# Kernel tuning notes

Measured on AMD Instinct MI355X. Metric: run time of the kernel, lower is better.

The kernel has to match this reference:

```python
import jax, jax.numpy as jnp
import numpy as np

N, H, F, E, K = 2048, 1024, 4096, 8, 2


def setup_inputs() -> dict:
    key = jax.random.key(0)
    ks = jax.random.split(key, 6)
    x = jax.random.normal(ks[0], (N, H), dtype=jnp.float32)
    mapping = jax.random.randint(ks[1], (N, K), 0, E)
    Wg = jax.random.normal(ks[2], (E, H), dtype=jnp.float32) * (1.0 / np.sqrt(H))
    W1 = jax.random.normal(ks[3], (E, H, F), dtype=jnp.float32) * (1.0 / np.sqrt(H))
    b1 = jnp.zeros((E, F), dtype=jnp.float32)
    W2 = jax.random.normal(ks[4], (E, F, H), dtype=jnp.float32) * (1.0 / np.sqrt(F))
    b2 = jnp.zeros((E, H), dtype=jnp.float32)
    return {"x": x, "mapping": mapping, "Wg": Wg, "W1": W1, "b1": b1, "W2": W2, "b2": b2}


def reference(x, mapping, Wg, W1, b1, W2, b2):
    # Gate logits: note original applies softmax over dim=0 (the token axis).
    logits = jax.nn.softmax(x @ Wg.T, axis=0)  # [N, E]

    # Per-expert MLP. Original sorts tokens by expert, runs per-expert GEMMs on
    # dynamic splits, then unsorts -- mathematically: y[i,k] = MLP_{mapping[i,k]}(x[i]).
    # JIT-friendly dense baseline: run every expert over all tokens, gather per token.
    def mlp(e):
        h = jax.nn.gelu(x @ W1[e] + b1[e])  # [N, F]
        return h @ W2[e] + b2[e]            # [N, H]

    y_all = jnp.stack([mlp(e) for e in range(E)])  # [E, N, H]

    # Gate weights gathered per (token, k), normalized over top-k.
    w = jnp.take_along_axis(logits, mapping, axis=1)  # [N, K]
    w = w / jnp.sum(w, axis=-1, keepdims=True)

    idx = jnp.arange(x.shape[0])
    out = jnp.zeros_like(x)
    for k in range(mapping.shape[1]):
        yk = y_all[mapping[:, k], idx]  # [N, H] gather per token's k-th expert
        out = out + yk * w[:, k:k + 1]
    return out
```

## Files before the change

### kernel.cpp

```cpp
#include <hip/hip_runtime.h>

#define N_TOK 2048
#define HD    1024
#define FD    4096
#define NE    8

typedef __attribute__((ext_vector_type(8))) short short8;
typedef __attribute__((ext_vector_type(4))) float floatx4;

__device__ __forceinline__ unsigned short f2bf(float f) {
  unsigned int u = __float_as_uint(f);
  u += 0x7fffu + ((u >> 16) & 1u);
  return (unsigned short)(u >> 16);
}

__device__ __forceinline__ void gl2lds16(const unsigned short* g, unsigned short* l) {
  __builtin_amdgcn_global_load_lds(
      (const __attribute__((address_space(1))) unsigned int*)g,
      (__attribute__((address_space(3))) unsigned int*)l, 16, 0, 0);
}

__device__ __forceinline__ float gelu_tanh(float x) {
  float t = 0.7978845608028654f * x * (1.0f + 0.044715f * x * x);
  return 0.5f * x * (1.0f + tanhf(t));
}

__device__ __forceinline__ int poff_of(const int* __restrict__ cnt, int e) {
  int o = 0;
  for (int i = 0; i < e; ++i) o += (cnt[i] + 127) & ~127;
  return o;
}

__global__ void k_gating(const float* __restrict__ x, const float* __restrict__ wg,
                         float* __restrict__ p) {
  int wave = threadIdx.x >> 6;
  int lane = threadIdx.x & 63;
  int n = blockIdx.x * 4 + wave;
  const float4* xr = (const float4*)(x + (size_t)n * HD);
  float4 xv[4];
  #pragma unroll
  for (int i = 0; i < 4; ++i) xv[i] = xr[lane + i * 64];
  for (int e = 0; e < NE; ++e) {
    const float4* wr = (const float4*)(wg + (size_t)e * HD);
    float s = 0.f;
    #pragma unroll
    for (int i = 0; i < 4; ++i) {
      float4 w4 = wr[lane + i * 64];
      s += xv[i].x * w4.x + xv[i].y * w4.y + xv[i].z * w4.z + xv[i].w * w4.w;
    }
    for (int o = 32; o > 0; o >>= 1) s += __shfl_xor(s, o, 64);
    if (lane == 0) p[e * N_TOK + n] = s;
  }
}

__global__ void k_softmax(float* __restrict__ p) {
  int e = blockIdx.x;
  float* col = p + e * N_TOK;
  __shared__ float red[256];
  int t = threadIdx.x;
  float m = -1e30f;
  for (int i = t; i < N_TOK; i += 256) m = fmaxf(m, col[i]);
  red[t] = m; __syncthreads();
  for (int s = 128; s > 0; s >>= 1) { if (t < s) red[t] = fmaxf(red[t], red[t + s]); __syncthreads(); }
  m = red[0]; __syncthreads();
  float sum = 0.f;
  for (int i = t; i < N_TOK; i += 256) { float v = expf(col[i] - m); col[i] = v; sum += v; }
  red[t] = sum; __syncthreads();
  for (int s = 128; s > 0; s >>= 1) { if (t < s) red[t] += red[t + s]; __syncthreads(); }
  float inv = 1.0f / red[0];
  for (int i = t; i < N_TOK; i += 256) col[i] *= inv;
}

__global__ void k_route(const int* __restrict__ mp, const float* __restrict__ p,
                        int* __restrict__ cnt, int* __restrict__ idxl,
                        int* __restrict__ tke, int* __restrict__ tks, float* __restrict__ tkw) {
  int n = blockIdx.x * 256 + threadIdx.x;
  if (n >= N_TOK) return;
  int m0 = mp[n * 2 + 0], m1 = mp[n * 2 + 1];
  if (m0 == m1) {
    int s = atomicAdd(&cnt[m0], 1);
    idxl[m0 * N_TOK + s] = n;
    tke[n * 2] = m0; tks[n * 2] = s; tkw[n * 2] = 1.0f;
    tke[n * 2 + 1] = m0; tks[n * 2 + 1] = s; tkw[n * 2 + 1] = 0.0f;
  } else {
    float p0 = p[m0 * N_TOK + n], p1 = p[m1 * N_TOK + n];
    float inv = 1.0f / (p0 + p1);
    int s0 = atomicAdd(&cnt[m0], 1);
    idxl[m0 * N_TOK + s0] = n;
    tke[n * 2] = m0; tks[n * 2] = s0; tkw[n * 2] = p0 * inv;
    int s1 = atomicAdd(&cnt[m1], 1);
    idxl[m1 * N_TOK + s1] = n;
    tke[n * 2 + 1] = m1; tks[n * 2 + 1] = s1; tkw[n * 2 + 1] = p1 * inv;
  }
}

__global__ void k_gather(const float* __restrict__ x, const int* __restrict__ cnt,
                         const int* __restrict__ idxl, unsigned short* __restrict__ xg) {
  int e = blockIdx.y;
  int r = blockIdx.x;
  int c = cnt[e];
  int pc = (c + 127) & ~127;
  if (r >= pc) return;
  unsigned short* dst = xg + ((size_t)poff_of(cnt, e) + r) * HD;
  int t = threadIdx.x;
  union { unsigned short us[8]; uint4 v; } o;
  if (r < c) {
    const float* src = x + (size_t)idxl[e * N_TOK + r] * HD;
    float4 f0 = ((const float4*)src)[t * 2];
    float4 f1 = ((const float4*)src)[t * 2 + 1];
    o.us[0] = f2bf(f0.x); o.us[1] = f2bf(f0.y); o.us[2] = f2bf(f0.z); o.us[3] = f2bf(f0.w);
    o.us[4] = f2bf(f1.x); o.us[5] = f2bf(f1.y); o.us[6] = f2bf(f1.z); o.us[7] = f2bf(f1.w);
  } else {
    o.v.x = 0u; o.v.y = 0u; o.v.z = 0u; o.v.w = 0u;
  }
  ((uint4*)dst)[t] = o.v;
}

__global__ __launch_bounds__(256) void k_transcvt2(const float* __restrict__ w1,
                                                   unsigned short* __restrict__ w1t,
                                                   const float* __restrict__ w2,
                                                   unsigned short* __restrict__ w2t) {
  __shared__ float tile[64][65];
  int l = blockIdx.x;
  const float* src; unsigned short* dst; int rows, cols, bx, by, e;
  if (l < 8192) {
    src = w1; dst = w1t; rows = HD; cols = FD;
    bx = l & 63; by = (l >> 6) & 15; e = l >> 10;
  } else {
    int l2 = l - 8192;
    src = w2; dst = w2t; rows = FD; cols = HD;
    bx = l2 & 15; by = (l2 >> 4) & 63; e = l2 >> 10;
  }
  const size_t base = (size_t)e * rows * cols;
  int c0 = bx * 64, r0 = by * 64;
  int t = threadIdx.x;
  int lr = t >> 4;
  int lc = (t & 15) * 4;
  #pragma unroll
  for (int i = 0; i < 64; i += 16) {
    float4 v = *(const float4*)(src + base + (size_t)(r0 + lr + i) * cols + c0 + lc);
    tile[lr + i][lc] = v.x; tile[lr + i][lc + 1] = v.y;
    tile[lr + i][lc + 2] = v.z; tile[lr + i][lc + 3] = v.w;
  }
  __syncthreads();
  int oc = t >> 2;
  int rseg = (t & 3) * 16;
  union { unsigned short us[16]; uint4 v[2]; } o;
  #pragma unroll
  for (int i = 0; i < 16; ++i) o.us[i] = f2bf(tile[rseg + i][oc]);
  unsigned short* d = dst + base + (size_t)(c0 + oc) * rows + r0 + rseg;
  ((uint4*)d)[0] = o.v[0];
  ((uint4*)d)[1] = o.v[1];
}

__global__ __launch_bounds__(256) void k_gemm1(
    const unsigned short* __restrict__ xg, const unsigned short* __restrict__ w1t,
    const float* __restrict__ b1, const int* __restrict__ cnt,
    unsigned short* __restrict__ h) {
  const int l = blockIdx.x;
  const int r = l & 7;
  const int m = (l >> 3) & 31;
  const int q = l >> 8;
  const int e = q >> 2;
  const int n = ((q & 3) << 3) | r;

  const int c = cnt[e];
  const int mbase = m * 64;
  if (mbase >= c) return;
  const int nbase = n * 128;
  const int po = poff_of(cnt, e);
  const unsigned short* A = xg + ((size_t)po + mbase) * HD;
  const unsigned short* B = w1t + ((size_t)e * FD + nbase) * HD;

  __shared__ unsigned short As[64 * 32];
  __shared__ unsigned short Bs[128 * 32];

  const int tid = threadIdx.x;
  const int wave = tid >> 6, lane = tid & 63;
  const int quad = lane >> 4, lrow = lane & 15;
  const int wn = wave * 32;

  floatx4 acc[4][2];
  #pragma unroll
  for (int i = 0; i < 4; ++i)
    #pragma unroll
    for (int j = 0; j < 2; ++j) acc[i][j] = (floatx4){0.f, 0.f, 0.f, 0.f};

  const int rA = tid >> 2, kA = (tid & 3) * 8;
  const int rB0 = tid >> 2, kB0 = (tid & 3) * 8;
  const int rB1 = (256 + tid) >> 2, kB1 = ((256 + tid) & 3) * 8;

  for (int kt = 0; kt < HD / 32; ++kt) {
    __syncthreads();
    const unsigned short* ga = A + kt * 32;
    const unsigned short* gb = B + kt * 32;
    gl2lds16(ga + (size_t)rA * HD + kA, As + (size_t)(wave * 64) * 8);
    gl2lds16(gb + (size_t)rB0 * HD + kB0, Bs + (size_t)(wave * 64) * 8);
    gl2lds16(gb + (size_t)rB1 * HD + kB1, Bs + (size_t)(256 + wave * 64) * 8);
    __syncthreads();
    short8 aF[4], bF[2];
    #pragma unroll
    for (int i = 0; i < 4; ++i) aF[i] = *(const short8*)(As + (i * 16 + lrow) * 32 + quad * 8);
    #pragma unroll
    for (int j = 0; j < 2; ++j) bF[j] = *(const short8*)(Bs + (wn + j * 16 + lrow) * 32 + quad * 8);
    #pragma unroll
    for (int i = 0; i < 4; ++i)
      #pragma unroll
      for (int j = 0; j < 2; ++j)
        acc[i][j] = __builtin_amdgcn_mfma_f32_16x16x32_bf16(aF[i], bF[j], acc[i][j], 0, 0, 0);
  }

  const size_t hrow0 = (size_t)po + mbase;
  #pragma unroll
  for (int i = 0; i < 4; ++i) {
    #pragma unroll
    for (int rr = 0; rr < 4; ++rr) {
      int row = i * 16 + quad * 4 + rr;
      unsigned short* hr = h + (hrow0 + row) * FD + nbase;
      #pragma unroll
      for (int j = 0; j < 2; ++j) {
        int col = wn + j * 16 + lrow;
        float v = acc[i][j][rr] + b1[e * FD + nbase + col];
        hr[col] = f2bf(gelu_tanh(v));
      }
    }
  }
}

__global__ __launch_bounds__(256) void k_gemm2(
    const unsigned short* __restrict__ h, const unsigned short* __restrict__ w2t,
    const int* __restrict__ cnt, unsigned short* __restrict__ ya) {
  const int l = blockIdx.x;
  const int nt = l & 15;
  const int mt = l >> 4;
  const int mbase = mt * 64;
  const int nbase = nt * 64;

  int e = -1, po = 0, ce = 0;
  {
    int o = 0;
    #pragma unroll
    for (int i = 0; i < NE; ++i) {
      int ci = cnt[i];
      int pc = (ci + 127) & ~127;
      if (mbase >= o && mbase < o + pc) { e = i; po = o; ce = ci; }
      o += pc;
    }
  }
  if (e < 0) return;
  if (mbase - po >= ce) return;

  const unsigned short* A = h + (size_t)mbase * FD;
  const unsigned short* B = w2t + ((size_t)e * HD + nbase) * FD;

  __shared__ unsigned short As[64 * 64];
  __shared__ unsigned short Bs[64 * 64];

  const int tid = threadIdx.x;
  const int wave = tid >> 6, lane = tid & 63;
  const int quad = lane >> 4, lrow = lane & 15;
  const int wm = (wave >> 1) * 32, wn = (wave & 1) * 32;

  floatx4 acc[2][2];
  #pragma unroll
  for (int i = 0; i < 2; ++i)
    #pragma unroll
    for (int j = 0; j < 2; ++j) acc[i][j] = (floatx4){0.f, 0.f, 0.f, 0.f};

  const int s0 = tid,        r0 = s0 >> 3, k0 = (s0 & 7) * 8;
  const int s1 = 256 + tid,  r1 = s1 >> 3, k1 = (s1 & 7) * 8;

  for (int kt = 0; kt < FD / 64; ++kt) {
    __syncthreads();
    const unsigned short* ga = A + kt * 64;
    const unsigned short* gb = B + kt * 64;
    gl2lds16(ga + (size_t)r0 * FD + k0, As + (size_t)(wave * 64) * 8);
    gl2lds16(ga + (size_t)r1 * FD + k1, As + (size_t)(256 + wave * 64) * 8);
    gl2lds16(gb + (size_t)r0 * FD + k0, Bs + (size_t)(wave * 64) * 8);
    gl2lds16(gb + (size_t)r1 * FD + k1, Bs + (size_t)(256 + wave * 64) * 8);
    __syncthreads();
    #pragma unroll
    for (int c = 0; c < 2; ++c) {
      short8 aF[2], bF[2];
      #pragma unroll
      for (int i = 0; i < 2; ++i) aF[i] = *(const short8*)(As + (wm + i * 16 + lrow) * 64 + c * 32 + quad * 8);
      #pragma unroll
      for (int j = 0; j < 2; ++j) bF[j] = *(const short8*)(Bs + (wn + j * 16 + lrow) * 64 + c * 32 + quad * 8);
      #pragma unroll
      for (int i = 0; i < 2; ++i)
        #pragma unroll
        for (int j = 0; j < 2; ++j)
          acc[i][j] = __builtin_amdgcn_mfma_f32_16x16x32_bf16(aF[i], bF[j], acc[i][j], 0, 0, 0);
    }
  }

  #pragma unroll
  for (int i = 0; i < 2; ++i) {
    #pragma unroll
    for (int rr = 0; rr < 4; ++rr) {
      int row = mbase + wm + i * 16 + quad * 4 + rr;
      unsigned short* yr = ya + (size_t)row * HD + nbase;
      #pragma unroll
      for (int j = 0; j < 2; ++j) {
        int col = wn + j * 16 + lrow;
        yr[col] = f2bf(acc[i][j][rr]);
      }
    }
  }
}

__global__ __launch_bounds__(256) void k_combine(
    const unsigned short* __restrict__ ya, const float* __restrict__ b2,
    const int* __restrict__ cnt, const int* __restrict__ tke,
    const int* __restrict__ tks, const float* __restrict__ tkw,
    float* __restrict__ out) {
  int n = blockIdx.x;
  int e0 = tke[n * 2], e1 = tke[n * 2 + 1];
  int p0 = poff_of(cnt, e0) + tks[n * 2];
  int p1 = poff_of(cnt, e1) + tks[n * 2 + 1];
  float w0 = tkw[n * 2], w1 = tkw[n * 2 + 1];
  int c = threadIdx.x * 4;
  union { unsigned short us[4]; ushort2 u2[2]; unsigned long long ll; } y0, y1;
  y0.ll = *(const unsigned long long*)(ya + (size_t)p0 * HD + c);
  y1.ll = *(const unsigned long long*)(ya + (size_t)p1 * HD + c);
  float4 bb0 = *(const float4*)(b2 + (size_t)e0 * HD + c);
  float4 bb1 = *(const float4*)(b2 + (size_t)e1 * HD + c);
  float4 o;
  o.x = w0 * (__uint_as_float((unsigned)y0.us[0] << 16) + bb0.x) + w1 * (__uint_as_float((unsigned)y1.us[0] << 16) + bb1.x);
  o.y = w0 * (__uint_as_float((unsigned)y0.us[1] << 16) + bb0.y) + w1 * (__uint_as_float((unsigned)y1.us[1] << 16) + bb1.y);
  o.z = w0 * (__uint_as_float((unsigned)y0.us[2] << 16) + bb0.z) + w1 * (__uint_as_float((unsigned)y1.us[2] << 16) + bb1.z);
  o.w = w0 * (__uint_as_float((unsigned)y0.us[3] << 16) + bb0.w) + w1 * (__uint_as_float((unsigned)y1.us[3] << 16) + bb1.w);
  *(float4*)(out + (size_t)n * HD + c) = o;
}

extern "C" void kernel_launch(void* const* d_in, const int* in_sizes, int n_in,
                              void* d_out, int out_size, void* d_ws, size_t ws_size,
                              hipStream_t stream) {
  const float* x  = (const float*)d_in[0];
  const int*   mp = (const int*)d_in[1];
  const float* wg = (const float*)d_in[2];
  const float* w1 = (const float*)d_in[3];
  const float* b1 = (const float*)d_in[4];
  const float* w2 = (const float*)d_in[5];
  const float* b2 = (const float*)d_in[6];
  float* out = (float*)d_out;
  char* ws = (char*)d_ws;

  float* p    = (float*)(ws + 0);
  int*   cnt  = (int*)(ws + 65536);
  int*   idxl = (int*)(ws + 66048);
  int*   tke  = (int*)(ws + 131584);
  int*   tks  = (int*)(ws + 147968);
  float* tkw  = (float*)(ws + 164352);
  size_t off = 180736;
  unsigned short* w1t = (unsigned short*)(ws + off);  off += 67108864;
  unsigned short* w2t = (unsigned short*)(ws + off);  off += 67108864;
  unsigned short* xg  = (unsigned short*)(ws + off);  off += 10485760;
  unsigned short* h   = (unsigned short*)(ws + off);  off += 41943040;
  unsigned short* ya  = (unsigned short*)(ws + off);  off += 10485760;

  hipMemsetAsync(cnt, 0, 32, stream);

  k_gating<<<512, 256, 0, stream>>>(x, wg, p);
  k_softmax<<<NE, 256, 0, stream>>>(p);
  k_route<<<NE, 256, 0, stream>>>(mp, p, cnt, idxl, tke, tks, tkw);
  k_transcvt2<<<16384, 256, 0, stream>>>(w1, w1t, w2, w2t);
  k_gather<<<dim3(N_TOK, NE), 128, 0, stream>>>(x, cnt, idxl, xg);
  k_gemm1<<<8192, 256, 0, stream>>>(xg, w1t, b1, cnt, h);
  k_gemm2<<<80 * 16, 256, 0, stream>>>(h, w2t, cnt, ya);
  k_combine<<<N_TOK, 256, 0, stream>>>(ya, b2, cnt, tke, tks, tkw, out);
}
```

Baseline: 505.1 us.

## Fuse weight transpose-convert and token gather into the expert GEMMs

Drops the separate kernel that transposed and converted W1/W2 to bf16 and the gather kernel. The GEMMs now read fp32 weights directly, convert them to bf16 while staging into padded LDS, and gather token rows by index from a bf16 copy of x made in the gating kernel. GEMM2 is also retiled to 64x128 to match GEMM1. This saves a full pass over 256MB of weights, but each weight tile is now reread as fp32 by every M-tile block, and the GEMMs take on the conversion work and non-async loads.

```diff
diff --git a/kernel.cpp b/kernel.cpp
--- a/kernel.cpp
+++ b/kernel.cpp
@@ -14,6 +14,10 @@
   return (unsigned short)(u >> 16);
 }
 
+__device__ __forceinline__ unsigned int pack2bf(float a, float b) {
+  return (unsigned int)f2bf(a) | ((unsigned int)f2bf(b) << 16);
+}
+
 __device__ __forceinline__ void gl2lds16(const unsigned short* g, unsigned short* l) {
   __builtin_amdgcn_global_load_lds(
       (const __attribute__((address_space(1))) unsigned int*)g,
@@ -31,8 +35,8 @@
   return o;
 }
 
-__global__ void k_gating(const float* __restrict__ x, const float* __restrict__ wg,
-                         float* __restrict__ p) {
+__global__ void k_gate_cvt(const float* __restrict__ x, const float* __restrict__ wg,
+                           float* __restrict__ p, unsigned short* __restrict__ xb) {
   int wave = threadIdx.x >> 6;
   int lane = threadIdx.x & 63;
   int n = blockIdx.x * 4 + wave;
@@ -40,6 +44,14 @@
   float4 xv[4];
   #pragma unroll
   for (int i = 0; i < 4; ++i) xv[i] = xr[lane + i * 64];
+  unsigned short* xrow = xb + (size_t)n * HD;
+  #pragma unroll
+  for (int i = 0; i < 4; ++i) {
+    uint2 w;
+    w.x = pack2bf(xv[i].x, xv[i].y);
+    w.y = pack2bf(xv[i].z, xv[i].w);
+    *(uint2*)(xrow + 4 * (lane + 64 * i)) = w;
+  }
   for (int e = 0; e < NE; ++e) {
     const float4* wr = (const float4*)(wg + (size_t)e * HD);
     float s = 0.f;
@@ -94,69 +106,10 @@
   }
 }
 
-__global__ void k_gather(const float* __restrict__ x, const int* __restrict__ cnt,
-                         const int* __restrict__ idxl, unsigned short* __restrict__ xg) {
-  int e = blockIdx.y;
-  int r = blockIdx.x;
-  int c = cnt[e];
-  int pc = (c + 127) & ~127;
-  if (r >= pc) return;
-  unsigned short* dst = xg + ((size_t)poff_of(cnt, e) + r) * HD;
-  int t = threadIdx.x;
-  union { unsigned short us[8]; uint4 v; } o;
-  if (r < c) {
-    const float* src = x + (size_t)idxl[e * N_TOK + r] * HD;
-    float4 f0 = ((const float4*)src)[t * 2];
-    float4 f1 = ((const float4*)src)[t * 2 + 1];
-    o.us[0] = f2bf(f0.x); o.us[1] = f2bf(f0.y); o.us[2] = f2bf(f0.z); o.us[3] = f2bf(f0.w);
-    o.us[4] = f2bf(f1.x); o.us[5] = f2bf(f1.y); o.us[6] = f2bf(f1.z); o.us[7] = f2bf(f1.w);
-  } else {
-    o.v.x = 0u; o.v.y = 0u; o.v.z = 0u; o.v.w = 0u;
-  }
-  ((uint4*)dst)[t] = o.v;
-}
-
-__global__ __launch_bounds__(256) void k_transcvt2(const float* __restrict__ w1,
-                                                   unsigned short* __restrict__ w1t,
-                                                   const float* __restrict__ w2,
-                                                   unsigned short* __restrict__ w2t) {
-  __shared__ float tile[64][65];
-  int l = blockIdx.x;
-  const float* src; unsigned short* dst; int rows, cols, bx, by, e;
-  if (l < 8192) {
-    src = w1; dst = w1t; rows = HD; cols = FD;
-    bx = l & 63; by = (l >> 6) & 15; e = l >> 10;
-  } else {
-    int l2 = l - 8192;
-    src = w2; dst = w2t; rows = FD; cols = HD;
-    bx = l2 & 15; by = (l2 >> 4) & 63; e = l2 >> 10;
-  }
-  const size_t base = (size_t)e * rows * cols;
-  int c0 = bx * 64, r0 = by * 64;
-  int t = threadIdx.x;
-  int lr = t >> 4;
-  int lc = (t & 15) * 4;
-  #pragma unroll
-  for (int i = 0; i < 64; i += 16) {
-    float4 v = *(const float4*)(src + base + (size_t)(r0 + lr + i) * cols + c0 + lc);
-    tile[lr + i][lc] = v.x; tile[lr + i][lc + 1] = v.y;
-    tile[lr + i][lc + 2] = v.z; tile[lr + i][lc + 3] = v.w;
-  }
-  __syncthreads();
-  int oc = t >> 2;
-  int rseg = (t & 3) * 16;
-  union { unsigned short us[16]; uint4 v[2]; } o;
-  #pragma unroll
-  for (int i = 0; i < 16; ++i) o.us[i] = f2bf(tile[rseg + i][oc]);
-  unsigned short* d = dst + base + (size_t)(c0 + oc) * rows + r0 + rseg;
-  ((uint4*)d)[0] = o.v[0];
-  ((uint4*)d)[1] = o.v[1];
-}
-
 __global__ __launch_bounds__(256) void k_gemm1(
-    const unsigned short* __restrict__ xg, const unsigned short* __restrict__ w1t,
+    const unsigned short* __restrict__ xb, const float* __restrict__ w1,
     const float* __restrict__ b1, const int* __restrict__ cnt,
-    unsigned short* __restrict__ h) {
+    const int* __restrict__ idxl, unsigned short* __restrict__ h) {
   const int l = blockIdx.x;
   const int r = l & 7;
   const int m = (l >> 3) & 31;
@@ -169,40 +122,53 @@
   if (mbase >= c) return;
   const int nbase = n * 128;
   const int po = poff_of(cnt, e);
-  const unsigned short* A = xg + ((size_t)po + mbase) * HD;
-  const unsigned short* B = w1t + ((size_t)e * FD + nbase) * HD;
 
   __shared__ unsigned short As[64 * 32];
-  __shared__ unsigned short Bs[128 * 32];
+  __shared__ unsigned short Bs[128 * 36];
 
   const int tid = threadIdx.x;
   const int wave = tid >> 6, lane = tid & 63;
   const int quad = lane >> 4, lrow = lane & 15;
   const int wn = wave * 32;
 
+  const int rA = tid >> 2, kA = (tid & 3) * 8;
+  const int tokA = idxl[e * N_TOK + min(mbase + rA, c - 1)];
+  const unsigned short* gArow = xb + (size_t)tokA * HD + kA;
+
+  const int kg = tid & 7, nc = tid >> 3;
+  const int k0 = kg * 4, n0 = nc * 4;
+  const float* gB = w1 + ((size_t)e * HD) * FD + (size_t)k0 * FD + nbase + n0;
+
   floatx4 acc[4][2];
   #pragma unroll
   for (int i = 0; i < 4; ++i)
     #pragma unroll
     for (int j = 0; j < 2; ++j) acc[i][j] = (floatx4){0.f, 0.f, 0.f, 0.f};
-
-  const int rA = tid >> 2, kA = (tid & 3) * 8;
-  const int rB0 = tid >> 2, kB0 = (tid & 3) * 8;
-  const int rB1 = (256 + tid) >> 2, kB1 = ((256 + tid) & 3) * 8;
 
   for (int kt = 0; kt < HD / 32; ++kt) {
     __syncthreads();
-    const unsigned short* ga = A + kt * 32;
-    const unsigned short* gb = B + kt * 32;
-    gl2lds16(ga + (size_t)rA * HD + kA, As + (size_t)(wave * 64) * 8);
-    gl2lds16(gb + (size_t)rB0 * HD + kB0, Bs + (size_t)(wave * 64) * 8);
-    gl2lds16(gb + (size_t)rB1 * HD + kB1, Bs + (size_t)(256 + wave * 64) * 8);
+    gl2lds16(gArow + kt * 32, As + (size_t)(wave * 64) * 8);
+    float4 wv[4];
+    const float* gBk = gB + (size_t)kt * 32 * FD;
+    #pragma unroll
+    for (int rr = 0; rr < 4; ++rr) wv[rr] = *(const float4*)(gBk + (size_t)rr * FD);
+    #pragma unroll
+    for (int i = 0; i < 4; ++i) {
+      float v0 = (&wv[0].x)[i], v1 = (&wv[1].x)[i], v2 = (&wv[2].x)[i], v3 = (&wv[3].x)[i];
+      uint2 wpk; wpk.x = pack2bf(v0, v1); wpk.y = pack2bf(v2, v3);
+      *(uint2*)(Bs + (n0 + i) * 36 + k0) = wpk;
+    }
     __syncthreads();
     short8 aF[4], bF[2];
     #pragma unroll
     for (int i = 0; i < 4; ++i) aF[i] = *(const short8*)(As + (i * 16 + lrow) * 32 + quad * 8);
     #pragma unroll
-    for (int j = 0; j < 2; ++j) bF[j] = *(const short8*)(Bs + (wn + j * 16 + lrow) * 32 + quad * 8);
+    for (int j = 0; j < 2; ++j) {
+      union { short8 v; uint2 u[2]; } bb;
+      const uint2* bp = (const uint2*)(Bs + (wn + j * 16 + lrow) * 36 + quad * 8);
+      bb.u[0] = bp[0]; bb.u[1] = bp[1];
+      bF[j] = bb.v;
+    }
     #pragma unroll
     for (int i = 0; i < 4; ++i)
       #pragma unroll
@@ -228,13 +194,13 @@
 }
 
 __global__ __launch_bounds__(256) void k_gemm2(
-    const unsigned short* __restrict__ h, const unsigned short* __restrict__ w2t,
+    const unsigned short* __restrict__ h, const float* __restrict__ w2,
     const int* __restrict__ cnt, unsigned short* __restrict__ ya) {
   const int l = blockIdx.x;
-  const int nt = l & 15;
-  const int mt = l >> 4;
+  const int n = l & 7;
+  const int mt = l >> 3;
   const int mbase = mt * 64;
-  const int nbase = nt * 64;
+  const int nbase = n * 128;
 
   int e = -1, po = 0, ce = 0;
   {
@@ -250,55 +216,63 @@
   if (e < 0) return;
   if (mbase - po >= ce) return;
 
-  const unsigned short* A = h + (size_t)mbase * FD;
-  const unsigned short* B = w2t + ((size_t)e * HD + nbase) * FD;
-
-  __shared__ unsigned short As[64 * 64];
-  __shared__ unsigned short Bs[64 * 64];
+  __shared__ unsigned short As[64 * 32];
+  __shared__ unsigned short Bs[128 * 36];
 
   const int tid = threadIdx.x;
   const int wave = tid >> 6, lane = tid & 63;
   const int quad = lane >> 4, lrow = lane & 15;
-  const int wm = (wave >> 1) * 32, wn = (wave & 1) * 32;
-
-  floatx4 acc[2][2];
-  #pragma unroll
-  for (int i = 0; i < 2; ++i)
+  const int wn = wave * 32;
+
+  const int rA = tid >> 2, kA = (tid & 3) * 8;
+  const unsigned short* gArow = h + (size_t)(mbase + rA) * FD + kA;
+
+  const int kg = tid & 7, nc = tid >> 3;
+  const int k0 = kg * 4, n0 = nc * 4;
+  const float* gB = w2 + ((size_t)e * FD) * HD + (size_t)k0 * HD + nbase + n0;
+
+  floatx4 acc[4][2];
+  #pragma unroll
+  for (int i = 0; i < 4; ++i)
     #pragma unroll
     for (int j = 0; j < 2; ++j) acc[i][j] = (floatx4){0.f, 0.f, 0.f, 0.f};
 
-  const int s0 = tid,        r0 = s0 >> 3, k0 = (s0 & 7) * 8;
-  const int s1 = 256 + tid,  r1 = s1 >> 3, k1 = (s1 & 7) * 8;
-
-  for (int kt = 0; kt < FD / 64; ++kt) {
+  for (int kt = 0; kt < FD / 32; ++kt) {
     __syncthreads();
-    const unsigned short* ga = A + kt * 64;
-    const unsigned short* gb = B + kt * 64;
-    gl2lds16(ga + (size_t)r0 * FD + k0, As + (size_t)(wave * 64) * 8);
-    gl2lds16(ga + (size_t)r1 * FD + k1, As + (size_t)(256 + wave * 64) * 8);
-    gl2lds16(gb + (size_t)r0 * FD + k0, Bs + (size_t)(wave * 64) * 8);
-    gl2lds16(gb + (size_t)r1 * FD + k1, Bs + (size_t)(256 + wave * 64) * 8);
+    gl2lds16(gArow + kt * 32, As + (size_t)(wave * 64) * 8);
+    float4 wv[4];
+    const float* gBk = gB + (size_t)kt * 32 * HD;
+    #pragma unroll
+    for (int rr = 0; rr < 4; ++rr) wv[rr] = *(const float4*)(gBk + (size_t)rr * HD);
+    #pragma unroll
+    for (int i = 0; i < 4; ++i) {
+      float v0 = (&wv[0].x)[i], v1 = (&wv[1].x)[i], v2 = (&wv[2].x)[i], v3 = (&wv[3].x)[i];
+      uint2 wpk; wpk.x = pack2bf(v0, v1); wpk.y = pack2bf(v2, v3);
+      *(uint2*)(Bs + (n0 + i) * 36 + k0) = wpk;
+    }
     __syncthreads();
-    #pragma unroll
-    for (int c = 0; c < 2; ++c) {
-      short8 aF[2], bF[2];
+    short8 aF[4], bF[2];
+    #pragma unroll
+    for (int i = 0; i < 4; ++i) aF[i] = *(const short8*)(As + (i * 16 + lrow) * 32 + quad * 8);
+    #pragma unroll
+    for (int j = 0; j < 2; ++j) {
+      union { short8 v; uint2 u[2]; } bb;
+      const uint2* bp = (const uint2*)(Bs + (wn + j * 16 + lrow) * 36 + quad * 8);
+      bb.u[0] = bp[0]; bb.u[1] = bp[1];
+      bF[j] = bb.v;
+    }
+    #pragma unroll
+    for (int i = 0; i < 4; ++i)
       #pragma unroll
-      for (int i = 0; i < 2; ++i) aF[i] = *(const short8*)(As + (wm + i * 16 + lrow) * 64 + c * 32 + quad * 8);
-      #pragma unroll
-      for (int j = 0; j < 2; ++j) bF[j] = *(const short8*)(Bs + (wn + j * 16 + lrow) * 64 + c * 32 + quad * 8);
-      #pragma unroll
-      for (int i = 0; i < 2; ++i)
-        #pragma unroll
-        for (int j = 0; j < 2; ++j)
-          acc[i][j] = __builtin_amdgcn_mfma_f32_16x16x32_bf16(aF[i], bF[j], acc[i][j], 0, 0, 0);
-    }
-  }
-
-  #pragma unroll
-  for (int i = 0; i < 2; ++i) {
+      for (int j = 0; j < 2; ++j)
+        acc[i][j] = __builtin_amdgcn_mfma_f32_16x16x32_bf16(aF[i], bF[j], acc[i][j], 0, 0, 0);
+  }
+
+  #pragma unroll
+  for (int i = 0; i < 4; ++i) {
     #pragma unroll
     for (int rr = 0; rr < 4; ++rr) {
-      int row = mbase + wm + i * 16 + quad * 4 + rr;
+      int row = mbase + i * 16 + quad * 4 + rr;
       unsigned short* yr = ya + (size_t)row * HD + nbase;
       #pragma unroll
       for (int j = 0; j < 2; ++j) {
@@ -320,7 +294,7 @@
   int p1 = poff_of(cnt, e1) + tks[n * 2 + 1];
   float w0 = tkw[n * 2], w1 = tkw[n * 2 + 1];
   int c = threadIdx.x * 4;
-  union { unsigned short us[4]; ushort2 u2[2]; unsigned long long ll; } y0, y1;
+  union { unsigned short us[4]; unsigned long long ll; } y0, y1;
   y0.ll = *(const unsigned long long*)(ya + (size_t)p0 * HD + c);
   y1.ll = *(const unsigned long long*)(ya + (size_t)p1 * HD + c);
   float4 bb0 = *(const float4*)(b2 + (size_t)e0 * HD + c);
@@ -353,20 +327,16 @@
   int*   tks  = (int*)(ws + 147968);
   float* tkw  = (float*)(ws + 164352);
   size_t off = 180736;
-  unsigned short* w1t = (unsigned short*)(ws + off);  off += 67108864;
-  unsigned short* w2t = (unsigned short*)(ws + off);  off += 67108864;
-  unsigned short* xg  = (unsigned short*)(ws + off);  off += 10485760;
-  unsigned short* h   = (unsigned short*)(ws + off);  off += 41943040;
-  unsigned short* ya  = (unsigned short*)(ws + off);  off += 10485760;
+  unsigned short* xb = (unsigned short*)(ws + off);  off += (size_t)N_TOK * HD * 2;
+  unsigned short* h  = (unsigned short*)(ws + off);  off += (size_t)5120 * FD * 2;
+  unsigned short* ya = (unsigned short*)(ws + off);  off += (size_t)5120 * HD * 2;
 
   hipMemsetAsync(cnt, 0, 32, stream);
 
-  k_gating<<<512, 256, 0, stream>>>(x, wg, p);
+  k_gate_cvt<<<512, 256, 0, stream>>>(x, wg, p, xb);
   k_softmax<<<NE, 256, 0, stream>>>(p);
   k_route<<<NE, 256, 0, stream>>>(mp, p, cnt, idxl, tke, tks, tkw);
-  k_transcvt2<<<16384, 256, 0, stream>>>(w1, w1t, w2, w2t);
-  k_gather<<<dim3(N_TOK, NE), 128, 0, stream>>>(x, cnt, idxl, xg);
-  k_gemm1<<<8192, 256, 0, stream>>>(xg, w1t, b1, cnt, h);
-  k_gemm2<<<80 * 16, 256, 0, stream>>>(h, w2t, cnt, ya);
+  k_gemm1<<<8192, 256, 0, stream>>>(xb, w1, b1, cnt, idxl, h);
+  k_gemm2<<<80 * 8, 256, 0, stream>>>(h, w2, cnt, ya);
   k_combine<<<N_TOK, 256, 0, stream>>>(ya, b2, cnt, tke, tks, tkw, out);
 }
```

New measurement: 572.4 us. 13.3% more time.
